# Kernel tuning notes

Hardware: AMD Instinct MI355X
Metric: run time of the kernel (lower is better)

The kernel has to match this reference:

```python
import jax, jax.numpy as jnp
import numpy as np

N_NODES = 100000
NEG_SLOPE = 0.2


def _gatv2_layer(x, src, dst, Wl, Wr, att, Wres, b):
    # x: [N, Cin]; src/dst: [E] (edge j->i means src=j, dst=i, PyG convention)
    xl = x @ Wl                     # [N, Cout] source-side projection
    xr = x @ Wr                     # [N, Cout] target-side projection
    h = jax.nn.leaky_relu(xl[src] + xr[dst], NEG_SLOPE)   # [E, Cout]
    e = h @ att                                            # [E] attention logits
    # segment softmax over incoming edges of each dst node
    emax = jax.ops.segment_max(e, dst, num_segments=N_NODES)
    ex = jnp.exp(e - emax[dst])
    denom = jax.ops.segment_sum(ex, dst, num_segments=N_NODES)
    alpha = ex / jnp.maximum(denom[dst], 1e-16)            # [E]
    # scatter-aggregate messages (alpha * xl[src]) into dst nodes
    agg = jax.ops.segment_sum(alpha[:, None] * xl[src], dst, num_segments=N_NODES)
    # residual projection + bias (PyG GATv2Conv residual=True)
    return agg + x @ Wres + b


def setup_inputs() -> dict:
    key = jax.random.key(0)
    ks = jax.random.split(key, 12)
    C = 128
    E = 500000
    s = 1.0 / np.sqrt(C)
    inp = {
        "x": jax.random.normal(ks[0], (N_NODES, C), dtype=jnp.float32),
        "edge_index": jax.random.randint(ks[1], (2, E), 0, N_NODES, dtype=jnp.int32),
        "Wl1": jax.random.normal(ks[2], (C, C), dtype=jnp.float32) * s,
        "Wr1": jax.random.normal(ks[3], (C, C), dtype=jnp.float32) * s,
        "att1": jax.random.normal(ks[4], (C,), dtype=jnp.float32) * s,
        "Wres1": jax.random.normal(ks[5], (C, C), dtype=jnp.float32) * s,
        "b1": jnp.zeros((C,), dtype=jnp.float32),
        "Wl2": jax.random.normal(ks[6], (C, C), dtype=jnp.float32) * s,
        "Wr2": jax.random.normal(ks[7], (C, C), dtype=jnp.float32) * s,
        "att2": jax.random.normal(ks[8], (C,), dtype=jnp.float32) * s,
        "Wres2": jax.random.normal(ks[9], (C, C), dtype=jnp.float32) * s,
        "b2": jnp.zeros((C,), dtype=jnp.float32),
    }
    return inp


def reference(x, edge_index, Wl1, Wr1, att1, Wres1, b1, Wl2, Wr2, att2, Wres2, b2):
    src, dst = edge_index[0], edge_index[1]
    x = jax.nn.relu(_gatv2_layer(x, src, dst, Wl1, Wr1, att1, Wres1, b1))
    x = jax.nn.relu(_gatv2_layer(x, src, dst, Wl2, Wr2, att2, Wres2, b2))
    return x
```

## Files before the change

kernel.cpp:

```cpp
#include <hip/hip_runtime.h>
#include <math.h>

#define N_NODES 100000
#define CDIM 128
#define E_EDGES 500000
#define NEG_SLOPE 0.2f
#define SCAN_CHUNK 1024
#define SCAN_NB ((N_NODES + SCAN_CHUNK - 1) / SCAN_CHUNK)
#define NTILES ((N_NODES + 15) / 16)
#define NUNITS (2 * NTILES)

typedef __attribute__((ext_vector_type(8))) short short8;
typedef __attribute__((ext_vector_type(8))) unsigned short ushort8;
typedef __attribute__((ext_vector_type(4))) unsigned short u16x4;
typedef __attribute__((ext_vector_type(4))) float f32x4;

static __device__ __forceinline__ float bf2f(unsigned short u) {
    unsigned int t = ((unsigned int)u) << 16;
    return __builtin_bit_cast(float, t);
}
static __device__ __forceinline__ unsigned short f2bf(float f) {
    unsigned int u = __builtin_bit_cast(unsigned int, f);
    unsigned int r = (u + 0x7FFFu + ((u >> 16) & 1u)) >> 16;
    return (unsigned short)r;
}
static __device__ __forceinline__ int clampi(int v, int hi) {
    return v < 0 ? 0 : (v >= hi ? hi - 1 : v);
}
static __device__ __forceinline__ float lrelu(float v) {
    return v > 0.0f ? v : NEG_SLOPE * v;
}

static __device__ __forceinline__ void gload_lds16(const void* g, void* l) {
    __builtin_amdgcn_global_load_lds(
        (const __attribute__((address_space(1))) void*)g,
        (__attribute__((address_space(3))) void*)l, 16, 0, 0);
}

__global__ __launch_bounds__(256)
void pack_w_all(const float* __restrict__ W0, const float* __restrict__ W1,
                const float* __restrict__ W2, const float* __restrict__ W3,
                const float* __restrict__ W4, const float* __restrict__ W5,
                unsigned short* __restrict__ Wf) {
    const float* Wp[6] = {W0, W1, W2, W3, W4, W5};
    int mi  = blockIdx.x >> 3;
    int rem = ((blockIdx.x & 7) << 8) | threadIdx.x;
    const float* W = Wp[mi];
    int l = rem & 63, t = (rem >> 6) & 7, kk = rem >> 9;
    int m = l & 15, q = l >> 4;
    int j = t * 16 + m;
    int k0 = kk * 32 + q * 8;
    ushort8 o;
#pragma unroll
    for (int u = 0; u < 8; ++u) o[u] = f2bf(W[(k0 + u) * 128 + j]);
    *(ushort8*)(Wf + ((size_t)mi * 2048 + rem) * 8) = o;
}

template <bool XSPLIT>
__global__ __launch_bounds__(1024, 4)
void projS(const void* __restrict__ Xv,
           const unsigned short* __restrict__ Wf,
           const float* __restrict__ bias,
           unsigned short* __restrict__ Aout,
           unsigned short* __restrict__ Bout,
           unsigned short* __restrict__ Rbout,
           int n_units, int n_rows) {
    __shared__ char wlds[98304];
    const int tid  = threadIdx.x;
    const int wave = tid >> 6;
    const int lane = tid & 63;
    const int m = lane & 15, q = lane >> 4;

#pragma unroll
    for (int c = 0; c < 6; ++c) {
        const int base = c * 16384 + wave * 1024;
        gload_lds16((const char*)Wf + base + lane * 16, wlds + base);
    }
    __syncthreads();

    const int NW = (int)(gridDim.x << 4);
    const int gw = (int)blockIdx.x * 16 + wave;
    const int ulo = (int)(((long long)gw * n_units) / NW);
    const int uhi = (int)(((long long)(gw + 1) * n_units) / NW);

#pragma clang loop unroll(disable)
    for (int u = ulo; u < uhi; ++u) {
        const int t = u >> 1;
        const int h = u & 1;
        const int xrow = t * 16 + m;
        const int arow = xrow < n_rows ? xrow : n_rows - 1;

        short8 xh[4], xl_[4];
#pragma unroll
        for (int kk = 0; kk < 4; ++kk) {
            if (XSPLIT) {
                const float* xp = (const float*)Xv + (size_t)arow * CDIM + kk * 32 + q * 8;
                f32x4 x0 = *(const f32x4*)xp;
                f32x4 x1 = *(const f32x4*)(xp + 4);
#pragma unroll
                for (int j = 0; j < 4; ++j) {
                    unsigned short h0 = f2bf(x0[j]);
                    xh[kk][j] = (short)h0;
                    xl_[kk][j] = (short)f2bf(x0[j] - bf2f(h0));
                    unsigned short h1 = f2bf(x1[j]);
                    xh[kk][4 + j] = (short)h1;
                    xl_[kk][4 + j] = (short)f2bf(x1[j] - bf2f(h1));
                }
            } else {
                xh[kk] = *(const short8*)((const unsigned short*)Xv +
                                          (size_t)arow * CDIM + kk * 32 + q * 8);
            }
        }

        f32x4 acc[3][4];
#pragma unroll
        for (int mi = 0; mi < 3; ++mi)
#pragma unroll
            for (int tt = 0; tt < 4; ++tt) acc[mi][tt] = (f32x4)0.0f;

#pragma unroll
        for (int kk = 0; kk < 4; ++kk) {
#pragma unroll
            for (int tt = 0; tt < 4; ++tt) {
                const int fo = ((kk * 8 + h * 4 + tt) * 64 + lane) * 16;
                short8 w0 = *(const short8*)(wlds + fo);
                short8 w1 = *(const short8*)(wlds + 32768 + fo);
                short8 w2 = *(const short8*)(wlds + 65536 + fo);
                acc[0][tt] = __builtin_amdgcn_mfma_f32_16x16x32_bf16(w0, xh[kk], acc[0][tt], 0, 0, 0);
                acc[1][tt] = __builtin_amdgcn_mfma_f32_16x16x32_bf16(w1, xh[kk], acc[1][tt], 0, 0, 0);
                acc[2][tt] = __builtin_amdgcn_mfma_f32_16x16x32_bf16(w2, xh[kk], acc[2][tt], 0, 0, 0);
                if (XSPLIT) {
                    acc[0][tt] = __builtin_amdgcn_mfma_f32_16x16x32_bf16(w0, xl_[kk], acc[0][tt], 0, 0, 0);
                    acc[1][tt] = __builtin_amdgcn_mfma_f32_16x16x32_bf16(w1, xl_[kk], acc[1][tt], 0, 0, 0);
                    acc[2][tt] = __builtin_amdgcn_mfma_f32_16x16x32_bf16(w2, xl_[kk], acc[2][tt], 0, 0, 0);
                }
            }
        }

        if (xrow < n_rows) {
#pragma unroll
            for (int tt = 0; tt < 4; ++tt) {
                const int tcol = h * 4 + tt;
                u16x4 oa, ob, orr;
                f32x4 bv = *(const f32x4*)(bias + tcol * 16 + q * 4);
#pragma unroll
                for (int r = 0; r < 4; ++r) {
                    oa[r] = f2bf(acc[0][tt][r]);
                    ob[r] = f2bf(acc[1][tt][r]);
                    orr[r] = f2bf(acc[2][tt][r] + bv[r]);
                }
                *(u16x4*)(Aout  + (size_t)xrow * CDIM + tcol * 16 + q * 4) = oa;
                *(u16x4*)(Bout  + (size_t)xrow * CDIM + tcol * 16 + q * 4) = ob;
                *(u16x4*)(Rbout + (size_t)xrow * CDIM + tcol * 16 + q * 4) = orr;
            }
        }
    }
}

__global__ __launch_bounds__(256)
void hist_dst(const int* __restrict__ dst, int* __restrict__ cnt, int n) {
    int e = blockIdx.x * 256 + threadIdx.x;
    if (e < n) atomicAdd(&cnt[clampi(dst[e], N_NODES)], 1);
}

__global__ __launch_bounds__(256)
void scan_local(const int* __restrict__ cnt, int* __restrict__ incl,
                int* __restrict__ blockSums, int n) {
    __shared__ int lds[256];
    int t = threadIdx.x;
    int base = blockIdx.x * SCAN_CHUNK + t * 4;
    int v[4], s = 0;
#pragma unroll
    for (int j = 0; j < 4; ++j) { v[j] = (base + j < n) ? cnt[base + j] : 0; s += v[j]; }
    lds[t] = s;
    __syncthreads();
    for (int off = 1; off < 256; off <<= 1) {
        int x = (t >= off) ? lds[t - off] : 0;
        __syncthreads();
        lds[t] += x;
        __syncthreads();
    }
    int run = lds[t] - s;
#pragma unroll
    for (int j = 0; j < 4; ++j) {
        run += v[j];
        if (base + j < n) incl[base + j] = run;
    }
    if (t == 255) blockSums[blockIdx.x] = lds[255];
}

__global__ __launch_bounds__(128)
void scan_sums(int* __restrict__ blockSums, int nb) {
    __shared__ int lds[128];
    int t = threadIdx.x;
    int v = (t < nb) ? blockSums[t] : 0;
    lds[t] = v;
    __syncthreads();
    for (int off = 1; off < 128; off <<= 1) {
        int x = (t >= off) ? lds[t - off] : 0;
        __syncthreads();
        lds[t] += x;
        __syncthreads();
    }
    if (t < nb) blockSums[t] = lds[t] - v;
}

__global__ __launch_bounds__(256)
void add_offsets(const int* __restrict__ incl, const int* __restrict__ blockSums,
                 const int* __restrict__ cnt, int* __restrict__ rowptr,
                 int* __restrict__ cursor, int n) {
    int i = blockIdx.x * 256 + threadIdx.x;
    if (i < n) {
        int v = incl[i] + blockSums[i / SCAN_CHUNK];
        rowptr[i + 1] = v;
        cursor[i] = v - cnt[i];
    }
    if (i == 0) rowptr[0] = 0;
}

__global__ __launch_bounds__(256)
void scatter_edges(const int* __restrict__ src, const int* __restrict__ dst,
                   int* __restrict__ cursor, int* __restrict__ esrc, int n) {
    int e = blockIdx.x * 256 + threadIdx.x;
    if (e < n) {
        int d = clampi(dst[e], N_NODES);
        int p = atomicAdd(&cursor[d], 1);
        esrc[p] = clampi(src[e], N_NODES);
    }
}

template <bool BF16OUT>
__global__ __launch_bounds__(256)
void fused_edge(const int* __restrict__ rowptr, const int* __restrict__ esrc,
                const unsigned short* __restrict__ A,
                const unsigned short* __restrict__ B,
                const float* __restrict__ att,
                const unsigned short* __restrict__ Rb, void* __restrict__ Outv,
                int n_nodes) {
    const int wave = threadIdx.x >> 6;
    const int lane = threadIdx.x & 63;
    const int g    = lane >> 4;
    const int i    = lane & 15;
    const int d    = (blockIdx.x * 4 + wave) * 4 + g;
    const bool valid = d < n_nodes;
    const int dd = valid ? d : n_nodes - 1;
    const int c0 = i * 8;

    ushort8 ub = *(const ushort8*)(B + (size_t)dd * CDIM + c0);
    float b[8], at[8];
    f32x4 at0 = *(const f32x4*)(att + c0);
    f32x4 at1 = *(const f32x4*)(att + c0 + 4);
#pragma unroll
    for (int j = 0; j < 4; ++j) {
        b[j] = bf2f(ub[j]);   b[4 + j] = bf2f(ub[4 + j]);
        at[j] = at0[j];       at[4 + j] = at1[j];
    }

    float acc[8] = {0, 0, 0, 0, 0, 0, 0, 0};
    float den = 0.0f;
    int p  = rowptr[dd];
    int p1 = valid ? rowptr[dd + 1] : p;

    for (; p < p1; ++p) {
        int s = esrc[p];
        ushort8 ua = *(const ushort8*)(A + (size_t)s * CDIM + c0);
        float a[8];
        float e = 0.0f;
#pragma unroll
        for (int j = 0; j < 8; ++j) {
            a[j] = bf2f(ua[j]);
            e += lrelu(a[j] + b[j]) * at[j];
        }
#pragma unroll
        for (int off = 8; off >= 1; off >>= 1) e += __shfl_xor(e, off, 16);
        float ee = __expf(fminf(e, 60.0f));
        den += ee;
#pragma unroll
        for (int j = 0; j < 8; ++j) acc[j] += ee * a[j];
    }

    if (valid) {
        float inv = 1.0f / fmaxf(den, 1e-16f);
        ushort8 rr = *(const ushort8*)(Rb + (size_t)d * CDIM + c0);
        float o[8];
#pragma unroll
        for (int j = 0; j < 8; ++j)
            o[j] = fmaxf(bf2f(rr[j]) + acc[j] * inv, 0.0f);
        if (BF16OUT) {
            ushort8 pk;
#pragma unroll
            for (int j = 0; j < 8; ++j) pk[j] = f2bf(o[j]);
            *(ushort8*)((unsigned short*)Outv + (size_t)d * CDIM + c0) = pk;
        } else {
            f32x4 o0, o1;
#pragma unroll
            for (int j = 0; j < 4; ++j) { o0[j] = o[j]; o1[j] = o[4 + j]; }
            float* op = (float*)Outv + (size_t)d * CDIM + c0;
            *(f32x4*)op = o0;
            *(f32x4*)(op + 4) = o1;
        }
    }
}

extern "C" void kernel_launch(void* const* d_in, const int* in_sizes, int n_in,
                              void* d_out, int out_size, void* d_ws, size_t ws_size,
                              hipStream_t stream) {
    const float* x     = (const float*)d_in[0];
    const int*   ei    = (const int*)d_in[1];
    const float* Wl1   = (const float*)d_in[2];
    const float* Wr1   = (const float*)d_in[3];
    const float* att1  = (const float*)d_in[4];
    const float* Wres1 = (const float*)d_in[5];
    const float* b1    = (const float*)d_in[6];
    const float* Wl2   = (const float*)d_in[7];
    const float* Wr2   = (const float*)d_in[8];
    const float* att2  = (const float*)d_in[9];
    const float* Wres2 = (const float*)d_in[10];
    const float* b2    = (const float*)d_in[11];

    const int* srcp = ei;
    const int* dstp = ei + E_EDGES;

    size_t off = 0;
    char* base = (char*)d_ws;
    auto carve = [&](size_t bytes) -> void* {
        void* q = base + off;
        off += (bytes + 255) & ~(size_t)255;
        return q;
    };
    unsigned short* Wf = (unsigned short*)carve((size_t)6 * 16384 * 2);
    unsigned short* A  = (unsigned short*)carve((size_t)N_NODES * CDIM * 2);
    unsigned short* B  = (unsigned short*)carve((size_t)N_NODES * CDIM * 2);
    unsigned short* X1 = (unsigned short*)carve((size_t)N_NODES * CDIM * 2);
    unsigned short* Rb = (unsigned short*)carve((size_t)N_NODES * CDIM * 2);
    int* cnt      = (int*)carve((size_t)N_NODES * 4);
    int* rowptr   = (int*)carve((size_t)(N_NODES + 1) * 4);
    int* cursor   = (int*)carve((size_t)N_NODES * 4);
    int* esrc     = (int*)carve((size_t)E_EDGES * 4);
    int* incl     = (int*)carve((size_t)N_NODES * 4);
    int* blockSums= (int*)carve((size_t)SCAN_NB * 4);
    (void)ws_size; (void)n_in; (void)in_sizes; (void)out_size;

    pack_w_all<<<48, 256, 0, stream>>>(Wl1, Wr1, Wres1, Wl2, Wr2, Wres2, Wf);

    (void)hipMemsetAsync(cnt, 0, (size_t)N_NODES * 4, stream);
    hist_dst<<<(E_EDGES + 255) / 256, 256, 0, stream>>>(dstp, cnt, E_EDGES);
    scan_local<<<SCAN_NB, 256, 0, stream>>>(cnt, incl, blockSums, N_NODES);
    scan_sums<<<1, 128, 0, stream>>>(blockSums, SCAN_NB);
    add_offsets<<<(N_NODES + 255) / 256, 256, 0, stream>>>(incl, blockSums, cnt,
                                                           rowptr, cursor, N_NODES);
    scatter_edges<<<(E_EDGES + 255) / 256, 256, 0, stream>>>(srcp, dstp, cursor,
                                                             esrc, E_EDGES);

    int egrid = (N_NODES + 15) / 16;

    projS<true ><<<256, 1024, 0, stream>>>(x, Wf, b1, A, B, Rb, NUNITS, N_NODES);
    fused_edge<true ><<<egrid, 256, 0, stream>>>(rowptr, esrc, A, B, att1, Rb, X1, N_NODES);
    projS<false><<<256, 1024, 0, stream>>>(X1, Wf + (size_t)3 * 16384, b2, A, B, Rb, NUNITS, N_NODES);
    fused_edge<false><<<egrid, 256, 0, stream>>>(rowptr, esrc, A, B, att2, Rb, d_out, N_NODES);
}
```

Measured before the change: 323.0 us.

## Prefetch next unit's X rows and split GEMM accumulators per output matrix

After: 318.4 us. No clear change (-1.4%).

```diff
diff --git a/kernel.cpp b/kernel.cpp
--- a/kernel.cpp
+++ b/kernel.cpp
@@ -82,21 +82,42 @@
     const int gw = (int)blockIdx.x * 16 + wave;
     const int ulo = (int)(((long long)gw * n_units) / NW);
     const int uhi = (int)(((long long)(gw + 1) * n_units) / NW);
+    if (ulo >= uhi) return;
+
+    f32x4  praw[8];
+    short8 braw[4];
+
+    {
+        const int t0 = ulo >> 1;
+        const int xr = t0 * 16 + m;
+        const int ar = xr < n_rows ? xr : n_rows - 1;
+        if (XSPLIT) {
+            const float* xp = (const float*)Xv + (size_t)ar * CDIM + q * 8;
+#pragma unroll
+            for (int kk = 0; kk < 4; ++kk) {
+                praw[2 * kk]     = *(const f32x4*)(xp + kk * 32);
+                praw[2 * kk + 1] = *(const f32x4*)(xp + kk * 32 + 4);
+            }
+        } else {
+            const unsigned short* xp = (const unsigned short*)Xv +
+                                       (size_t)ar * CDIM + q * 8;
+#pragma unroll
+            for (int kk = 0; kk < 4; ++kk) braw[kk] = *(const short8*)(xp + kk * 32);
+        }
+    }
 
 #pragma clang loop unroll(disable)
     for (int u = ulo; u < uhi; ++u) {
         const int t = u >> 1;
         const int h = u & 1;
         const int xrow = t * 16 + m;
-        const int arow = xrow < n_rows ? xrow : n_rows - 1;
 
         short8 xh[4], xl_[4];
 #pragma unroll
         for (int kk = 0; kk < 4; ++kk) {
             if (XSPLIT) {
-                const float* xp = (const float*)Xv + (size_t)arow * CDIM + kk * 32 + q * 8;
-                f32x4 x0 = *(const f32x4*)xp;
-                f32x4 x1 = *(const f32x4*)(xp + 4);
+                f32x4 x0 = praw[2 * kk];
+                f32x4 x1 = praw[2 * kk + 1];
 #pragma unroll
                 for (int j = 0; j < 4; ++j) {
                     unsigned short h0 = f2bf(x0[j]);
@@ -107,51 +128,64 @@
                     xl_[kk][4 + j] = (short)f2bf(x1[j] - bf2f(h1));
                 }
             } else {
-                xh[kk] = *(const short8*)((const unsigned short*)Xv +
-                                          (size_t)arow * CDIM + kk * 32 + q * 8);
-            }
-        }
-
-        f32x4 acc[3][4];
-#pragma unroll
-        for (int mi = 0; mi < 3; ++mi)
-#pragma unroll
-            for (int tt = 0; tt < 4; ++tt) acc[mi][tt] = (f32x4)0.0f;
-
-#pragma unroll
-        for (int kk = 0; kk < 4; ++kk) {
-#pragma unroll
-            for (int tt = 0; tt < 4; ++tt) {
-                const int fo = ((kk * 8 + h * 4 + tt) * 64 + lane) * 16;
-                short8 w0 = *(const short8*)(wlds + fo);
-                short8 w1 = *(const short8*)(wlds + 32768 + fo);
-                short8 w2 = *(const short8*)(wlds + 65536 + fo);
-                acc[0][tt] = __builtin_amdgcn_mfma_f32_16x16x32_bf16(w0, xh[kk], acc[0][tt], 0, 0, 0);
-                acc[1][tt] = __builtin_amdgcn_mfma_f32_16x16x32_bf16(w1, xh[kk], acc[1][tt], 0, 0, 0);
-                acc[2][tt] = __builtin_amdgcn_mfma_f32_16x16x32_bf16(w2, xh[kk], acc[2][tt], 0, 0, 0);
-                if (XSPLIT) {
-                    acc[0][tt] = __builtin_amdgcn_mfma_f32_16x16x32_bf16(w0, xl_[kk], acc[0][tt], 0, 0, 0);
-                    acc[1][tt] = __builtin_amdgcn_mfma_f32_16x16x32_bf16(w1, xl_[kk], acc[1][tt], 0, 0, 0);
-                    acc[2][tt] = __builtin_amdgcn_mfma_f32_16x16x32_bf16(w2, xl_[kk], acc[2][tt], 0, 0, 0);
+                xh[kk] = braw[kk];
+            }
+        }
+
+        {
+            const int un = (u + 1 < uhi) ? u + 1 : u;
+            const int tn = un >> 1;
+            const int xr = tn * 16 + m;
+            const int ar = xr < n_rows ? xr : n_rows - 1;
+            if (XSPLIT) {
+                const float* xp = (const float*)Xv + (size_t)ar * CDIM + q * 8;
+#pragma unroll
+                for (int kk = 0; kk < 4; ++kk) {
+                    praw[2 * kk]     = *(const f32x4*)(xp + kk * 32);
+                    praw[2 * kk + 1] = *(const f32x4*)(xp + kk * 32 + 4);
                 }
-            }
-        }
-
-        if (xrow < n_rows) {
-#pragma unroll
-            for (int tt = 0; tt < 4; ++tt) {
-                const int tcol = h * 4 + tt;
-                u16x4 oa, ob, orr;
-                f32x4 bv = *(const f32x4*)(bias + tcol * 16 + q * 4);
-#pragma unroll
-                for (int r = 0; r < 4; ++r) {
-                    oa[r] = f2bf(acc[0][tt][r]);
-                    ob[r] = f2bf(acc[1][tt][r]);
-                    orr[r] = f2bf(acc[2][tt][r] + bv[r]);
+            } else {
+                const unsigned short* xp = (const unsigned short*)Xv +
+                                           (size_t)ar * CDIM + q * 8;
+#pragma unroll
+                for (int kk = 0; kk < 4; ++kk) braw[kk] = *(const short8*)(xp + kk * 32);
+            }
+        }
+
+        unsigned short* const outs[3] = {Aout, Bout, Rbout};
+#pragma unroll
+        for (int mi = 0; mi < 3; ++mi) {
+            f32x4 acc[4];
+#pragma unroll
+            for (int tt = 0; tt < 4; ++tt) acc[tt] = (f32x4)0.0f;
+
+#pragma unroll
+            for (int kk = 0; kk < 4; ++kk) {
+#pragma unroll
+                for (int tt = 0; tt < 4; ++tt) {
+                    const int fo = ((kk * 8 + h * 4 + tt) * 64 + lane) * 16;
+                    short8 w = *(const short8*)(wlds + mi * 32768 + fo);
+                    acc[tt] = __builtin_amdgcn_mfma_f32_16x16x32_bf16(w, xh[kk], acc[tt], 0, 0, 0);
+                    if (XSPLIT)
+                        acc[tt] = __builtin_amdgcn_mfma_f32_16x16x32_bf16(w, xl_[kk], acc[tt], 0, 0, 0);
                 }
-                *(u16x4*)(Aout  + (size_t)xrow * CDIM + tcol * 16 + q * 4) = oa;
-                *(u16x4*)(Bout  + (size_t)xrow * CDIM + tcol * 16 + q * 4) = ob;
-                *(u16x4*)(Rbout + (size_t)xrow * CDIM + tcol * 16 + q * 4) = orr;
+            }
+
+            if (xrow < n_rows) {
+#pragma unroll
+                for (int tt = 0; tt < 4; ++tt) {
+                    const int tcol = h * 4 + tt;
+                    u16x4 o;
+                    if (mi == 2) {
+                        f32x4 bv = *(const f32x4*)(bias + tcol * 16 + q * 4);
+#pragma unroll
+                        for (int r = 0; r < 4; ++r) o[r] = f2bf(acc[tt][r] + bv[r]);
+                    } else {
+#pragma unroll
+                        for (int r = 0; r < 4; ++r) o[r] = f2bf(acc[tt][r]);
+                    }
+                    *(u16x4*)(outs[mi] + (size_t)xrow * CDIM + tcol * 16 + q * 4) = o;
+                }
             }
         }
     }
```
